# Kernel tuning notes

Measured on AMD Instinct MI355X. Metric: run time of the kernel, lower is better.

Reference implementation:

```python
import jax, jax.numpy as jnp
import numpy as np

B, N, CA, CS, CZ, H, NQ, NK = 2, 16384, 128, 128, 16, 4, 32, 128
DH = CA // H
NB = N // NQ


def _ln(x, gamma=None, eps=1e-5):
    m = jnp.mean(x, -1, keepdims=True)
    v = jnp.var(x, -1, keepdims=True)
    y = (x - m) * jax.lax.rsqrt(v + eps)
    return y if gamma is None else y * gamma


def _adaln(a, s, gamma_s, Wg, bg, Wskip):
    # AF3 Algorithm 26: LN(a) without affine; LN(s) with scale, no offset;
    # out = sigmoid(Linear(s)) * a + LinearNoBias(s)
    a_n = _ln(a)
    s_n = _ln(s, gamma_s)
    return jax.nn.sigmoid(s_n @ Wg + bg) * a_n + s_n @ Wskip


def setup_inputs():
    key = jax.random.key(0)
    ks = jax.random.split(key, 20)
    def nrm(i, shape, scale=0.02):
        return jax.random.normal(ks[i], shape, jnp.float32) * scale
    return {
        "a": jax.random.normal(ks[0], (B, N, CA), jnp.float32),
        "s": jax.random.normal(ks[1], (B, N, CS), jnp.float32),
        "z": jax.random.normal(ks[2], (B, NB, NQ, NK, CZ), jnp.float32),
        "apb_gamma_s": jnp.ones((CS,), jnp.float32),
        "apb_Wg": nrm(3, (CS, CA)),
        "apb_bg": jnp.zeros((CA,), jnp.float32),
        "apb_Wskip": nrm(4, (CS, CA)),
        "Wq": nrm(5, (CA, CA)), "bq": jnp.zeros((CA,), jnp.float32),
        "Wk": nrm(6, (CA, CA)), "Wv": nrm(7, (CA, CA)),
        "Wgate": nrm(8, (CA, CA)), "Wo": nrm(9, (CA, CA)),
        "gamma_z": jnp.ones((CZ,), jnp.float32),
        "Wz": nrm(10, (CZ, H)),
        "Ws_last": nrm(11, (CS, CA)),
        "bs_last": jnp.full((CA,), -2.0, jnp.float32),
        "ct_gamma_s": jnp.ones((CS,), jnp.float32),
        "ct_Wg": nrm(12, (CS, CA)), "ct_bg": jnp.zeros((CA,), jnp.float32),
        "ct_Wskip": nrm(13, (CS, CA)),
        "Wa1": nrm(14, (CA, 2 * CA)), "Wa2": nrm(15, (CA, 2 * CA)),
        "Wb": nrm(16, (2 * CA, CA)),
        "Ws": nrm(17, (CS, CA)), "bs": jnp.full((CA,), -2.0, jnp.float32),
        "n_queries": NQ, "n_keys": NK,
    }


def reference(a, s, z, apb_gamma_s, apb_Wg, apb_bg, apb_Wskip, Wq, bq, Wk, Wv,
              Wgate, Wo, gamma_z, Wz, Ws_last, bs_last, ct_gamma_s, ct_Wg,
              ct_bg, ct_Wskip, Wa1, Wa2, Wb, Ws, bs, n_queries, n_keys):
    nq, nk = int(n_queries), int(n_keys)
    nb = N // nq
    # ---- AttentionPairBias, local windowed attention ----
    a1 = _adaln(a, s, apb_gamma_s, apb_Wg, apb_bg, apb_Wskip)  # [B,N,CA]
    # trunked pair bias: [B,nb,nq,nk,H] -> [B,H,nb,nq,nk]
    bias = jnp.transpose(_ln(z, gamma_z) @ Wz, (0, 4, 1, 2, 3))
    q = (a1 @ Wq + bq).reshape(B, N, H, DH).transpose(0, 2, 1, 3)
    k = (a1 @ Wk).reshape(B, N, H, DH).transpose(0, 2, 1, 3)
    v = (a1 @ Wv).reshape(B, N, H, DH).transpose(0, 2, 1, 3)
    qb = q.reshape(B, H, nb, nq, DH)
    pad = (nk - nq) // 2
    # centered key window per query block
    idx = (jnp.arange(nb) * nq - pad)[:, None] + jnp.arange(nk)[None, :]  # [nb,nk]
    valid = (idx >= 0) & (idx < N)
    idxc = jnp.clip(idx, 0, N - 1)
    kb = k[:, :, idxc]  # [B,H,nb,nk,DH]
    vb = v[:, :, idxc]
    scores = jnp.einsum('bhnqd,bhnkd->bhnqk', qb, kb) / np.sqrt(DH).astype(np.float32) + bias
    scores = jnp.where(valid[None, None, :, None, :], scores, -1e9)
    attn = jax.nn.softmax(scores, axis=-1)
    o = jnp.einsum('bhnqk,bhnkd->bhnqd', attn, vb)  # [B,H,nb,nq,DH]
    o = o.reshape(B, H, N, DH).transpose(0, 2, 1, 3).reshape(B, N, CA)
    g = jax.nn.sigmoid(a1 @ Wgate)  # per-channel gating
    attn_out = (g * o) @ Wo
    b_out = jax.nn.sigmoid(s @ Ws_last + bs_last) * attn_out
    # ---- ConditionedTransitionBlock (Alg 25) ----
    a3 = _adaln(a, s, ct_gamma_s, ct_Wg, ct_bg, ct_Wskip)
    t = jax.nn.silu(a3 @ Wa1) * (a3 @ Wa2)
    ct_out = jax.nn.sigmoid(s @ Ws + bs) * (t @ Wb)
    # Alg 23: a = b + ConditionedTransitionBlock(a, s)
    return b_out + ct_out
```

## Files before the change

kernel.cpp:

```cpp
#include <hip/hip_runtime.h>

typedef _Float16 f16;
typedef f16 f16x8 __attribute__((ext_vector_type(8)));
typedef f16 f16x4 __attribute__((ext_vector_type(4)));
typedef f16 f16x2 __attribute__((ext_vector_type(2)));
typedef float f32x4 __attribute__((ext_vector_type(4)));

#define MFMA16(a,b,c) __builtin_amdgcn_mfma_f32_16x16x32_f16((a),(b),(c),0,0,0)

static __device__ __forceinline__ f16x8 ld8(const f16* p){ return *(const f16x8*)p; }
static __device__ __forceinline__ float sigm(float x){ return 1.f/(1.f + __expf(-x)); }

__global__ __launch_bounds__(256) void k_prep(
    const float* __restrict__ apb_gamma, const float* __restrict__ apb_Wg, const float* __restrict__ apb_Wskip,
    const float* __restrict__ ct_gamma,  const float* __restrict__ ct_Wg,  const float* __restrict__ ct_Wskip,
    const float* __restrict__ Wq, const float* __restrict__ Wk, const float* __restrict__ Wv, const float* __restrict__ Wgate,
    const float* __restrict__ Wsl, const float* __restrict__ Wss,
    const float* __restrict__ Wa1, const float* __restrict__ Wa2,
    const float* __restrict__ Wo, const float* __restrict__ Wb,
    const float* __restrict__ gamma_z, const float* __restrict__ Wz,
    f16* __restrict__ wA, f16* __restrict__ wC, f16* __restrict__ wQK, f16* __restrict__ wVG,
    f16* __restrict__ wSG, f16* __restrict__ wAB, f16* __restrict__ wO, f16* __restrict__ wBt,
    float* __restrict__ wzg, float* __restrict__ Slv, float* __restrict__ Ssv)
{
  const int t0 = blockIdx.x*256 + threadIdx.x;
  const int stride = gridDim.x*256;
  for (int i = t0; i < 256*128; i += stride){
    const int n = i >> 7, k = i & 127;
    const int m = n & 127;
    wA[i]  = (f16)(((n<128) ? apb_Wg[k*128+m] : apb_Wskip[k*128+m]) * apb_gamma[k]);
    wC[i]  = (f16)(((n<128) ? ct_Wg[k*128+m]  : ct_Wskip[k*128+m])  * ct_gamma[k]);
    wQK[i] = (f16)((n<128) ? Wq[k*128+m] : Wk[k*128+m]);
    wVG[i] = (f16)((n<128) ? Wv[k*128+m] : Wgate[k*128+m]);
    wSG[i] = (f16)((n<128) ? Wsl[k*128+m] : Wss[k*128+m]);
  }
  for (int i = t0; i < 512*128; i += stride){
    const int n = i >> 7, k = i & 127;
    wAB[i] = (f16)((n < 256) ? Wa1[k*256 + n] : Wa2[k*256 + (n-256)]);
  }
  for (int i = t0; i < 128*128; i += stride){
    const int n = i >> 7, k = i & 127;
    wO[i] = (f16)Wo[k*128+n];
  }
  for (int i = t0; i < 128*256; i += stride){
    const int n = i >> 8, k = i & 255;
    wBt[i] = (f16)Wb[k*128+n];
  }
  if (t0 < 64) wzg[t0] = gamma_z[t0 & 15] * Wz[(t0 & 15)*4 + (t0 >> 4)];
  if (t0 < 256){
    const int cc = t0 & 127;
    const float* Wp = (t0 >= 128) ? Wss : Wsl;
    float acc = 0.f;
    for (int k = 0; k < 128; k++) acc += Wp[k*128 + cc];
    if (t0 >= 128) Ssv[cc] = acc; else Slv[cc] = acc;
  }
}

__global__ __launch_bounds__(256) void k_pre(
    const float* __restrict__ A, const float* __restrict__ S,
    const f16* __restrict__ wA, const f16* __restrict__ wC,
    const f16* __restrict__ wQK, const f16* __restrict__ wVG,
    const f16* __restrict__ wSG, const f16* __restrict__ wAB,
    const float* __restrict__ bgA, const float* __restrict__ bgC,
    const float* __restrict__ bq, const float* __restrict__ bsl, const float* __restrict__ bss,
    const float* __restrict__ Slv, const float* __restrict__ Ssv,
    f16* __restrict__ Qo, f16* __restrict__ Ko, f16* __restrict__ Vt, f16* __restrict__ Go,
    f16* __restrict__ T, f16* __restrict__ GL, f16* __restrict__ GS)
{
  __shared__ f16 lsn[64*136];
  __shared__ f16 lan[64*136];
  __shared__ f16 la1[64*136];
  __shared__ f16 la3[64*136];
  __shared__ float lsm[64], lsd[64];
  const int tid = threadIdx.x;
  const size_t rbase = (size_t)blockIdx.x * 64;

  {
    const int row = tid >> 2, part = tid & 3;
    const size_t gr = rbase + row;
    {
      const float* sp = S + gr*128 + part*32;
      float v[32];
      #pragma unroll
      for (int j = 0; j < 8; j++){
        const float4 t4 = ((const float4*)sp)[j];
        v[j*4+0]=t4.x; v[j*4+1]=t4.y; v[j*4+2]=t4.z; v[j*4+3]=t4.w;
      }
      float sm = 0.f, sq = 0.f;
      #pragma unroll
      for (int j = 0; j < 32; j++){ sm += v[j]; sq += v[j]*v[j]; }
      sm += __shfl_xor(sm,1); sq += __shfl_xor(sq,1);
      sm += __shfl_xor(sm,2); sq += __shfl_xor(sq,2);
      const float mean = sm*(1.f/128.f);
      const float var  = sq*(1.f/128.f) - mean*mean;
      const float rstd = rsqrtf(var + 1e-5f);
      if (part == 0){ lsm[row] = mean; lsd[row] = (var + 1e-5f)*rstd; }
      #pragma unroll
      for (int j = 0; j < 4; j++){
        f16x8 o;
        #pragma unroll
        for (int e = 0; e < 8; e++) o[e] = (f16)((v[j*8+e]-mean)*rstd);
        *(f16x8*)&lsn[row*136 + part*32 + j*8] = o;
      }
    }
    {
      const float* ap = A + gr*128 + part*32;
      float v[32];
      #pragma unroll
      for (int j = 0; j < 8; j++){
        const float4 t4 = ((const float4*)ap)[j];
        v[j*4+0]=t4.x; v[j*4+1]=t4.y; v[j*4+2]=t4.z; v[j*4+3]=t4.w;
      }
      float sm = 0.f, sq = 0.f;
      #pragma unroll
      for (int j = 0; j < 32; j++){ sm += v[j]; sq += v[j]*v[j]; }
      sm += __shfl_xor(sm,1); sq += __shfl_xor(sq,1);
      sm += __shfl_xor(sm,2); sq += __shfl_xor(sq,2);
      const float mean = sm*(1.f/128.f);
      const float var  = sq*(1.f/128.f) - mean*mean;
      const float rstd = rsqrtf(var + 1e-5f);
      #pragma unroll
      for (int j = 0; j < 4; j++){
        f16x8 o;
        #pragma unroll
        for (int e = 0; e < 8; e++) o[e] = (f16)((v[j*8+e]-mean)*rstd);
        *(f16x8*)&lan[row*136 + part*32 + j*8] = o;
      }
    }
  }
  __syncthreads();

  const int l = tid & 63, w = tid >> 6;
  const int c = l & 15, q4 = l >> 4;

  for (int jj = 0; jj < 4; jj++){
    const int job = jj*4 + w;
    const int n0 = (job >> 1)*16;
    const int mat = job & 1;
    const f16* W = mat ? wC : wA;
    f16* dst = mat ? la3 : la1;
    const float bv = (mat ? bgC : bgA)[n0 + c];
    f16x8 b0[4], b1[4];
    #pragma unroll
    for (int kc = 0; kc < 4; kc++){
      b0[kc] = ld8(W + (size_t)(n0 + c)*128 + kc*32 + q4*8);
      b1[kc] = ld8(W + (size_t)(128 + n0 + c)*128 + kc*32 + q4*8);
    }
    for (int mi = 0; mi < 4; mi++){
      f32x4 d0 = {0,0,0,0}, d1 = {0,0,0,0};
      #pragma unroll
      for (int kc = 0; kc < 4; kc++){
        const f16x8 av = *(const f16x8*)&lsn[(mi*16 + c)*136 + kc*32 + q4*8];
        d0 = MFMA16(av, b0[kc], d0);
        d1 = MFMA16(av, b1[kc], d1);
      }
      #pragma unroll
      for (int r = 0; r < 4; r++){
        const int row = mi*16 + q4*4 + r;
        const float anv = (float)lan[row*136 + n0 + c];
        dst[row*136 + n0 + c] = (f16)(sigm(d0[r] + bv)*anv + d1[r]);
      }
    }
  }
  __syncthreads();

  for (int jj = 0; jj < 2; jj++){
    const int n0 = (jj*4 + w)*16;
    f16x8 bQ[4], bK[4], bV[4], bG[4];
    #pragma unroll
    for (int kc = 0; kc < 4; kc++){
      bQ[kc] = ld8(wQK + (size_t)(n0 + c)*128 + kc*32 + q4*8);
      bK[kc] = ld8(wQK + (size_t)(128 + n0 + c)*128 + kc*32 + q4*8);
      bV[kc] = ld8(wVG + (size_t)(n0 + c)*128 + kc*32 + q4*8);
      bG[kc] = ld8(wVG + (size_t)(128 + n0 + c)*128 + kc*32 + q4*8);
    }
    const float bvq = bq[n0 + c];
    for (int mi = 0; mi < 4; mi++){
      f32x4 dQ = {0,0,0,0}, dK = {0,0,0,0}, dV = {0,0,0,0}, dG = {0,0,0,0};
      #pragma unroll
      for (int kc = 0; kc < 4; kc++){
        const f16x8 av = *(const f16x8*)&la1[(mi*16 + c)*136 + kc*32 + q4*8];
        dQ = MFMA16(av, bQ[kc], dQ);
        dK = MFMA16(av, bK[kc], dK);
        dV = MFMA16(av, bV[kc], dV);
        dG = MFMA16(av, bG[kc], dG);
      }
      #pragma unroll
      for (int r = 0; r < 4; r++){
        const size_t grow = rbase + mi*16 + q4*4 + r;
        Qo[grow*128 + n0 + c] = (f16)((dQ[r] + bvq)*0.17677669529663687f);
        Ko[grow*128 + n0 + c] = (f16)dK[r];
        Go[grow*128 + n0 + c] = (f16)sigm(dG[r]);
      }
      f16x4 vv;
      #pragma unroll
      for (int r = 0; r < 4; r++) vv[r] = (f16)dV[r];
      const int bidx = (int)(rbase >> 14);
      const int ntk  = (int)(rbase & 16383) + mi*16 + q4*4;
      *(f16x4*)(Vt + ((size_t)bidx*128 + n0 + c)*16384 + ntk) = vv;
    }
  }

  for (int jj = 0; jj < 4; jj++){
    const int n0t = (jj*4 + w)*16;
    f16x8 b1v[4], b2v[4];
    #pragma unroll
    for (int kc = 0; kc < 4; kc++){
      b1v[kc] = ld8(wAB + (size_t)(n0t + c)*128 + kc*32 + q4*8);
      b2v[kc] = ld8(wAB + (size_t)(256 + n0t + c)*128 + kc*32 + q4*8);
    }
    for (int mi = 0; mi < 4; mi++){
      f32x4 d0 = {0,0,0,0}, d1 = {0,0,0,0};
      #pragma unroll
      for (int kc = 0; kc < 4; kc++){
        const f16x8 av = *(const f16x8*)&la3[(mi*16 + c)*136 + kc*32 + q4*8];
        d0 = MFMA16(av, b1v[kc], d0);
        d1 = MFMA16(av, b2v[kc], d1);
      }
      #pragma unroll
      for (int r = 0; r < 4; r++){
        const size_t grow = rbase + mi*16 + q4*4 + r;
        const float u = d0[r];
        T[grow*256 + n0t + c] = (f16)((u*sigm(u))*d1[r]);
      }
    }
  }

  for (int jj = 0; jj < 2; jj++){
    const int n0 = (jj*4 + w)*16;
    f16x8 b0[4], b1[4];
    #pragma unroll
    for (int kc = 0; kc < 4; kc++){
      b0[kc] = ld8(wSG + (size_t)(n0 + c)*128 + kc*32 + q4*8);
      b1[kc] = ld8(wSG + (size_t)(128 + n0 + c)*128 + kc*32 + q4*8);
    }
    const float slc = Slv[n0 + c], ssc = Ssv[n0 + c];
    const float bl = bsl[n0 + c],  bs2 = bss[n0 + c];
    for (int mi = 0; mi < 4; mi++){
      f32x4 d0 = {0,0,0,0}, d1 = {0,0,0,0};
      #pragma unroll
      for (int kc = 0; kc < 4; kc++){
        const f16x8 av = *(const f16x8*)&lsn[(mi*16 + c)*136 + kc*32 + q4*8];
        d0 = MFMA16(av, b0[kc], d0);
        d1 = MFMA16(av, b1[kc], d1);
      }
      #pragma unroll
      for (int r = 0; r < 4; r++){
        const int row = mi*16 + q4*4 + r;
        const size_t grow = rbase + row;
        const float mn = lsm[row], sd = lsd[row];
        GL[grow*128 + n0 + c] = (f16)sigm(d0[r]*sd + mn*slc + bl);
        GS[grow*128 + n0 + c] = (f16)sigm(d1[r]*sd + mn*ssc + bs2);
      }
    }
  }
}

__global__ __launch_bounds__(512) void k_attn(const f16* __restrict__ Q, const f16* __restrict__ K,
    const f16* __restrict__ VT, const float* __restrict__ Z, const float* __restrict__ WZG,
    f16* __restrict__ Og)
{
  __shared__ f16 upb[17408];
  __shared__ float wzg_s[64];
  const int tid = threadIdx.x;
  const int b = blockIdx.x >> 9, nb = blockIdx.x & 511;
  if (tid < 64) wzg_s[tid] = WZG[tid];
  __syncthreads();
  #pragma unroll
  for (int i = 0; i < 8; i++){
    const int p  = tid + i*512;
    const int qq = p >> 7, kk = p & 127;
    const float* zp = Z + ((((size_t)b*512 + nb)*32 + qq)*128 + kk)*16;
    const float4 z0 = *(const float4*)(zp);
    const float4 z1 = *(const float4*)(zp + 4);
    const float4 z2 = *(const float4*)(zp + 8);
    const float4 z3 = *(const float4*)(zp + 12);
    const float xs[16] = {z0.x,z0.y,z0.z,z0.w, z1.x,z1.y,z1.z,z1.w,
                          z2.x,z2.y,z2.z,z2.w, z3.x,z3.y,z3.z,z3.w};
    float sm = 0.f, sq = 0.f;
    #pragma unroll
    for (int cc = 0; cc < 16; cc++){ sm += xs[cc]; sq += xs[cc]*xs[cc]; }
    const float mean = sm*(1.f/16.f);
    const float var  = sq*(1.f/16.f) - mean*mean;
    const float rs   = rsqrtf(var + 1e-5f);
    #pragma unroll
    for (int h = 0; h < 4; h++){
      float acc = 0.f;
      #pragma unroll
      for (int cc = 0; cc < 16; cc++) acc += (xs[cc]-mean)*wzg_s[h*16+cc];
      upb[(h*32 + qq)*132 + kk] = (f16)(acc*rs);
    }
  }
  __syncthreads();

  const int l = tid & 63, w = tid >> 6;
  const int c = l & 15, q4 = l >> 4;
  const int h = w >> 1, qh = w & 1, m0 = qh*16;
  const f16x8 aq = ld8(Q + ((size_t)b*16384 + (size_t)nb*32 + m0 + c)*128 + h*32 + q4*8);
  const long kbase = (long)b*16384 + (long)nb*32 - 48;
  f32x4 sc[8];
  #pragma unroll
  for (int nt = 0; nt < 8; nt++){
    const f16x8 bf = ld8(K + (kbase + nt*16 + c)*128 + h*32 + q4*8);
    f32x4 zz = {0.f,0.f,0.f,0.f};
    sc[nt] = MFMA16(aq, bf, zz);
  }
  #pragma unroll
  for (int nt = 0; nt < 8; nt++){
    const int key = nt*16 + c;
    const long kt = (long)nb*32 - 48 + key;
    const bool inv = (kt < 0) || (kt >= 16384);
    #pragma unroll
    for (int r = 0; r < 4; r++){
      const float v = sc[nt][r] + (float)upb[(h*32 + m0 + q4*4 + r)*132 + key];
      sc[nt][r] = inv ? -1e9f : v;
    }
  }
  #pragma unroll
  for (int r = 0; r < 4; r++){
    float mx = sc[0][r];
    #pragma unroll
    for (int nt = 1; nt < 8; nt++) mx = fmaxf(mx, sc[nt][r]);
    #pragma unroll
    for (int o = 8; o; o >>= 1) mx = fmaxf(mx, __shfl_xor(mx, o));
    float sum = 0.f;
    #pragma unroll
    for (int nt = 0; nt < 8; nt++){ const float e = __expf(sc[nt][r]-mx); sc[nt][r] = e; sum += e; }
    #pragma unroll
    for (int o = 8; o; o >>= 1) sum += __shfl_xor(sum, o);
    const float inv = 1.f/sum;
    #pragma unroll
    for (int nt = 0; nt < 8; nt++) sc[nt][r] *= inv;
  }
  __syncthreads();
  #pragma unroll
  for (int nt = 0; nt < 8; nt++)
    #pragma unroll
    for (int r = 0; r < 4; r++)
      upb[(w*16 + q4*4 + r)*136 + nt*16 + c] = (f16)sc[nt][r];
  const f16* vb = VT + ((long)b*128)*16384 + (long)nb*32 - 48;
  f32x4 o0 = {0.f,0.f,0.f,0.f}, o1 = {0.f,0.f,0.f,0.f};
  #pragma unroll
  for (int kc = 0; kc < 4; kc++){
    const f16x8 pa = *(const f16x8*)&upb[(w*16 + c)*136 + kc*32 + q4*8];
    const f16x8 v0 = ld8(vb + (long)(h*32 + c)*16384 + kc*32 + q4*8);
    const f16x8 v1 = ld8(vb + (long)(h*32 + 16 + c)*16384 + kc*32 + q4*8);
    o0 = MFMA16(pa, v0, o0);
    o1 = MFMA16(pa, v1, o1);
  }
  #pragma unroll
  for (int r = 0; r < 4; r++){
    const size_t tok = (size_t)b*16384 + (size_t)nb*32 + m0 + q4*4 + r;
    Og[tok*128 + h*32 + c]      = (f16)o0[r];
    Og[tok*128 + h*32 + 16 + c] = (f16)o1[r];
  }
}

__global__ __launch_bounds__(256) void k_final(const f16* __restrict__ G, const f16* __restrict__ O,
    const f16* __restrict__ T, const f16* __restrict__ Wot, const f16* __restrict__ Wbt,
    const f16* __restrict__ GL, const f16* __restrict__ GS, float* __restrict__ out)
{
  const int l = threadIdx.x & 63, w = threadIdx.x >> 6;
  const int c = l & 15, q4 = l >> 4;
  const int mbase = blockIdx.x*64 + w*16;
  f16x8 ag[4], at[8];
  const f16* gp = G + (size_t)(mbase + c)*128 + q4*8;
  const f16* op = O + (size_t)(mbase + c)*128 + q4*8;
  #pragma unroll
  for (int kc = 0; kc < 4; kc++) ag[kc] = ld8(gp + kc*32) * ld8(op + kc*32);
  const f16* tp = T + (size_t)(mbase + c)*256 + q4*8;
  #pragma unroll
  for (int kc = 0; kc < 8; kc++) at[kc] = ld8(tp + kc*32);
  for (int nt = 0; nt < 8; nt++){
    const int cb = nt*16;
    f32x4 d1 = {0,0,0,0}, d2 = {0,0,0,0};
    #pragma unroll
    for (int kc = 0; kc < 4; kc++)
      d1 = MFMA16(ag[kc], ld8(Wot + (size_t)(cb + c)*128 + kc*32 + q4*8), d1);
    #pragma unroll
    for (int kc = 0; kc < 8; kc++)
      d2 = MFMA16(at[kc], ld8(Wbt + (size_t)(cb + c)*256 + kc*32 + q4*8), d2);
    #pragma unroll
    for (int r = 0; r < 4; r++){
      const size_t row = mbase + q4*4 + r;
      const float glv = (float)GL[row*128 + cb + c];
      const float gsv = (float)GS[row*128 + cb + c];
      out[row*128 + cb + c] = glv*d1[r] + gsv*d2[r];
    }
  }
}

extern "C" void kernel_launch(void* const* d_in, const int* in_sizes, int n_in,
                              void* d_out, int out_size, void* d_ws, size_t ws_size,
                              hipStream_t stream)
{
  (void)in_sizes; (void)n_in; (void)out_size; (void)ws_size;
  const float* a        = (const float*)d_in[0];
  const float* s        = (const float*)d_in[1];
  const float* z        = (const float*)d_in[2];
  const float* apb_gamma= (const float*)d_in[3];
  const float* apb_Wg   = (const float*)d_in[4];
  const float* apb_bg   = (const float*)d_in[5];
  const float* apb_Wskip= (const float*)d_in[6];
  const float* Wq       = (const float*)d_in[7];
  const float* bq       = (const float*)d_in[8];
  const float* Wk       = (const float*)d_in[9];
  const float* Wv       = (const float*)d_in[10];
  const float* Wgate    = (const float*)d_in[11];
  const float* Wo       = (const float*)d_in[12];
  const float* gamma_z  = (const float*)d_in[13];
  const float* Wz       = (const float*)d_in[14];
  const float* Wsl      = (const float*)d_in[15];
  const float* bsl      = (const float*)d_in[16];
  const float* ct_gamma = (const float*)d_in[17];
  const float* ct_Wg    = (const float*)d_in[18];
  const float* ct_bg    = (const float*)d_in[19];
  const float* ct_Wskip = (const float*)d_in[20];
  const float* Wa1      = (const float*)d_in[21];
  const float* Wa2      = (const float*)d_in[22];
  const float* Wb       = (const float*)d_in[23];
  const float* Wss      = (const float*)d_in[24];
  const float* bss      = (const float*)d_in[25];

  f16* W0 = (f16*)d_ws;
  const size_t SL = (size_t)32768*128;
  f16* qv = W0 + 0*SL;
  f16* kv = W0 + 1*SL;
  f16* vt = W0 + 2*SL;
  f16* gv = W0 + 3*SL;
  f16* tv = W0 + 4*SL;
  f16* gl = W0 + 6*SL;
  f16* gs = W0 + 7*SL;
  f16* ov = W0 + 8*SL;
  f16* wA  = W0 + 9*SL;
  f16* wC  = wA  + 256*128;
  f16* wQK = wC  + 256*128;
  f16* wVG = wQK + 256*128;
  f16* wSG = wVG + 256*128;
  f16* wAB = wSG + 256*128;
  f16* wO  = wAB + 512*128;
  f16* wBt = wO  + 128*128;
  float* wzg = (float*)(wBt + 128*256);
  float* Slv = wzg + 64;
  float* Ssv = Slv + 128;

  k_prep<<<dim3(64),256,0,stream>>>(apb_gamma,apb_Wg,apb_Wskip, ct_gamma,ct_Wg,ct_Wskip,
      Wq,Wk,Wv,Wgate, Wsl,Wss, Wa1,Wa2, Wo,Wb, gamma_z,Wz,
      wA,wC,wQK,wVG,wSG,wAB,wO,wBt,wzg,Slv,Ssv);
  k_pre<<<dim3(512),256,0,stream>>>(a,s, wA,wC,wQK,wVG,wSG,wAB,
      apb_bg,ct_bg,bq,bsl,bss,Slv,Ssv, qv,kv,vt,gv,tv,gl,gs);
  k_attn<<<dim3(1024),512,0,stream>>>(qv,kv,vt,z,wzg,ov);
  k_final<<<dim3(512),256,0,stream>>>(gv,ov,tv,wO,wBt,gl,gs,(float*)d_out);
}
```

Measured before the change: 534.9 us.

## Fuse output projection into attention kernel and trim k_pre shared memory

```diff
diff --git a/kernel.cpp b/kernel.cpp
--- a/kernel.cpp
+++ b/kernel.cpp
@@ -21,7 +21,8 @@
     const float* __restrict__ gamma_z, const float* __restrict__ Wz,
     f16* __restrict__ wA, f16* __restrict__ wC, f16* __restrict__ wQK, f16* __restrict__ wVG,
     f16* __restrict__ wSG, f16* __restrict__ wAB, f16* __restrict__ wO, f16* __restrict__ wBt,
-    float* __restrict__ wzg, float* __restrict__ Slv, float* __restrict__ Ssv)
+    float* __restrict__ wzg, float* __restrict__ Slv, float* __restrict__ Ssv,
+    float* __restrict__ wcs)
 {
   const int t0 = blockIdx.x*256 + threadIdx.x;
   const int stride = gridDim.x*256;
@@ -54,9 +55,14 @@
     for (int k = 0; k < 128; k++) acc += Wp[k*128 + cc];
     if (t0 >= 128) Ssv[cc] = acc; else Slv[cc] = acc;
   }
+  if (t0 < 4){
+    float acc = 0.f;
+    for (int cc = 0; cc < 16; cc++) acc += gamma_z[cc]*Wz[cc*4 + t0];
+    wcs[t0] = acc;
+  }
 }
 
-__global__ __launch_bounds__(256) void k_pre(
+__global__ __launch_bounds__(256,3) void k_pre(
     const float* __restrict__ A, const float* __restrict__ S,
     const f16* __restrict__ wA, const f16* __restrict__ wC,
     const f16* __restrict__ wQK, const f16* __restrict__ wVG,
@@ -67,10 +73,9 @@
     f16* __restrict__ Qo, f16* __restrict__ Ko, f16* __restrict__ Vt, f16* __restrict__ Go,
     f16* __restrict__ T, f16* __restrict__ GL, f16* __restrict__ GS)
 {
-  __shared__ f16 lsn[64*136];
-  __shared__ f16 lan[64*136];
-  __shared__ f16 la1[64*136];
-  __shared__ f16 la3[64*136];
+  __shared__ __attribute__((aligned(16))) f16 lsn[64*136];
+  __shared__ __attribute__((aligned(16))) f16 lan[64*136];
+  __shared__ __attribute__((aligned(16))) f16 la1[64*136];
   __shared__ float lsm[64], lsd[64];
   const int tid = threadIdx.x;
   const size_t rbase = (size_t)blockIdx.x * 64;
@@ -133,32 +138,33 @@
   const int l = tid & 63, w = tid >> 6;
   const int c = l & 15, q4 = l >> 4;
 
-  for (int jj = 0; jj < 4; jj++){
-    const int job = jj*4 + w;
-    const int n0 = (job >> 1)*16;
-    const int mat = job & 1;
-    const f16* W = mat ? wC : wA;
-    f16* dst = mat ? la3 : la1;
-    const float bv = (mat ? bgC : bgA)[n0 + c];
-    f16x8 b0[4], b1[4];
+  for (int jj = 0; jj < 2; jj++){
+    const int n0 = (jj*4 + w)*16;
+    const float bvA = bgA[n0 + c], bvC = bgC[n0 + c];
+    f16x8 bA0[4], bA1[4], bC0[4], bC1[4];
     #pragma unroll
     for (int kc = 0; kc < 4; kc++){
-      b0[kc] = ld8(W + (size_t)(n0 + c)*128 + kc*32 + q4*8);
-      b1[kc] = ld8(W + (size_t)(128 + n0 + c)*128 + kc*32 + q4*8);
+      bA0[kc] = ld8(wA + (size_t)(n0 + c)*128 + kc*32 + q4*8);
+      bA1[kc] = ld8(wA + (size_t)(128 + n0 + c)*128 + kc*32 + q4*8);
+      bC0[kc] = ld8(wC + (size_t)(n0 + c)*128 + kc*32 + q4*8);
+      bC1[kc] = ld8(wC + (size_t)(128 + n0 + c)*128 + kc*32 + q4*8);
     }
     for (int mi = 0; mi < 4; mi++){
-      f32x4 d0 = {0,0,0,0}, d1 = {0,0,0,0};
+      f32x4 dA0 = {0,0,0,0}, dA1 = {0,0,0,0}, dC0 = {0,0,0,0}, dC1 = {0,0,0,0};
       #pragma unroll
       for (int kc = 0; kc < 4; kc++){
         const f16x8 av = *(const f16x8*)&lsn[(mi*16 + c)*136 + kc*32 + q4*8];
-        d0 = MFMA16(av, b0[kc], d0);
-        d1 = MFMA16(av, b1[kc], d1);
+        dA0 = MFMA16(av, bA0[kc], dA0);
+        dA1 = MFMA16(av, bA1[kc], dA1);
+        dC0 = MFMA16(av, bC0[kc], dC0);
+        dC1 = MFMA16(av, bC1[kc], dC1);
       }
       #pragma unroll
       for (int r = 0; r < 4; r++){
         const int row = mi*16 + q4*4 + r;
         const float anv = (float)lan[row*136 + n0 + c];
-        dst[row*136 + n0 + c] = (f16)(sigm(d0[r] + bv)*anv + d1[r]);
+        la1[row*136 + n0 + c] = (f16)(sigm(dA0[r] + bvA)*anv + dA1[r]);
+        lan[row*136 + n0 + c] = (f16)(sigm(dC0[r] + bvC)*anv + dC1[r]);
       }
     }
   }
@@ -213,7 +219,7 @@
       f32x4 d0 = {0,0,0,0}, d1 = {0,0,0,0};
       #pragma unroll
       for (int kc = 0; kc < 4; kc++){
-        const f16x8 av = *(const f16x8*)&la3[(mi*16 + c)*136 + kc*32 + q4*8];
+        const f16x8 av = *(const f16x8*)&lan[(mi*16 + c)*136 + kc*32 + q4*8];
         d0 = MFMA16(av, b1v[kc], d0);
         d1 = MFMA16(av, b2v[kc], d1);
       }
@@ -256,15 +262,37 @@
   }
 }
 
-__global__ __launch_bounds__(512) void k_attn(const f16* __restrict__ Q, const f16* __restrict__ K,
+__global__ __launch_bounds__(512,2) void k_attn(const f16* __restrict__ Q, const f16* __restrict__ K,
     const f16* __restrict__ VT, const float* __restrict__ Z, const float* __restrict__ WZG,
-    f16* __restrict__ Og)
+    const float* __restrict__ WCS,
+    const f16* __restrict__ G, const f16* __restrict__ T,
+    const f16* __restrict__ GL, const f16* __restrict__ GS,
+    const f16* __restrict__ Wot, const f16* __restrict__ Wbt,
+    float* __restrict__ out)
 {
-  __shared__ f16 upb[17408];
+  __shared__ __attribute__((aligned(16))) f16 upb[17408];
+  __shared__ __attribute__((aligned(16))) f16 obuf[32*136];
   __shared__ float wzg_s[64];
+  __shared__ float wcs_s[4];
   const int tid = threadIdx.x;
   const int b = blockIdx.x >> 9, nb = blockIdx.x & 511;
   if (tid < 64) wzg_s[tid] = WZG[tid];
+  if (tid < 4)  wcs_s[tid] = WCS[tid];
+
+  const int l = tid & 63, w = tid >> 6;
+  const int c = l & 15, q4 = l >> 4;
+  const int h = w >> 1, qh = w & 1, m0 = qh*16;
+
+  const f16x8 aq = ld8(Q + ((size_t)b*16384 + (size_t)nb*32 + m0 + c)*128 + h*32 + q4*8);
+  const long kbase = (long)b*16384 + (long)nb*32 - 48;
+  f32x4 sc[8];
+  #pragma unroll
+  for (int nt = 0; nt < 8; nt++){
+    const f16x8 bf = ld8(K + (kbase + nt*16 + c)*128 + h*32 + q4*8);
+    f32x4 zz = {0.f,0.f,0.f,0.f};
+    sc[nt] = MFMA16(aq, bf, zz);
+  }
+
   __syncthreads();
   #pragma unroll
   for (int i = 0; i < 8; i++){
@@ -284,27 +312,15 @@
     const float var  = sq*(1.f/16.f) - mean*mean;
     const float rs   = rsqrtf(var + 1e-5f);
     #pragma unroll
-    for (int h = 0; h < 4; h++){
+    for (int hh = 0; hh < 4; hh++){
       float acc = 0.f;
       #pragma unroll
-      for (int cc = 0; cc < 16; cc++) acc += (xs[cc]-mean)*wzg_s[h*16+cc];
-      upb[(h*32 + qq)*132 + kk] = (f16)(acc*rs);
-    }
-  }
-  __syncthreads();
-
-  const int l = tid & 63, w = tid >> 6;
-  const int c = l & 15, q4 = l >> 4;
-  const int h = w >> 1, qh = w & 1, m0 = qh*16;
-  const f16x8 aq = ld8(Q + ((size_t)b*16384 + (size_t)nb*32 + m0 + c)*128 + h*32 + q4*8);
-  const long kbase = (long)b*16384 + (long)nb*32 - 48;
-  f32x4 sc[8];
-  #pragma unroll
-  for (int nt = 0; nt < 8; nt++){
-    const f16x8 bf = ld8(K + (kbase + nt*16 + c)*128 + h*32 + q4*8);
-    f32x4 zz = {0.f,0.f,0.f,0.f};
-    sc[nt] = MFMA16(aq, bf, zz);
-  }
+      for (int cc = 0; cc < 16; cc++) acc += xs[cc]*wzg_s[hh*16+cc];
+      upb[(hh*32 + qq)*132 + kk] = (f16)((acc - mean*wcs_s[hh])*rs);
+    }
+  }
+  __syncthreads();
+
   #pragma unroll
   for (int nt = 0; nt < 8; nt++){
     const int key = nt*16 + c;
@@ -338,6 +354,7 @@
     #pragma unroll
     for (int r = 0; r < 4; r++)
       upb[(w*16 + q4*4 + r)*136 + nt*16 + c] = (f16)sc[nt][r];
+
   const f16* vb = VT + ((long)b*128)*16384 + (long)nb*32 - 48;
   f32x4 o0 = {0.f,0.f,0.f,0.f}, o1 = {0.f,0.f,0.f,0.f};
   #pragma unroll
@@ -350,42 +367,37 @@
   }
   #pragma unroll
   for (int r = 0; r < 4; r++){
-    const size_t tok = (size_t)b*16384 + (size_t)nb*32 + m0 + q4*4 + r;
-    Og[tok*128 + h*32 + c]      = (f16)o0[r];
-    Og[tok*128 + h*32 + 16 + c] = (f16)o1[r];
-  }
-}
-
-__global__ __launch_bounds__(256) void k_final(const f16* __restrict__ G, const f16* __restrict__ O,
-    const f16* __restrict__ T, const f16* __restrict__ Wot, const f16* __restrict__ Wbt,
-    const f16* __restrict__ GL, const f16* __restrict__ GS, float* __restrict__ out)
-{
-  const int l = threadIdx.x & 63, w = threadIdx.x >> 6;
-  const int c = l & 15, q4 = l >> 4;
-  const int mbase = blockIdx.x*64 + w*16;
-  f16x8 ag[4], at[8];
-  const f16* gp = G + (size_t)(mbase + c)*128 + q4*8;
-  const f16* op = O + (size_t)(mbase + c)*128 + q4*8;
-  #pragma unroll
-  for (int kc = 0; kc < 4; kc++) ag[kc] = ld8(gp + kc*32) * ld8(op + kc*32);
-  const f16* tp = T + (size_t)(mbase + c)*256 + q4*8;
-  #pragma unroll
-  for (int kc = 0; kc < 8; kc++) at[kc] = ld8(tp + kc*32);
-  for (int nt = 0; nt < 8; nt++){
-    const int cb = nt*16;
+    obuf[(m0 + q4*4 + r)*136 + h*32 + c]      = (f16)o0[r];
+    obuf[(m0 + q4*4 + r)*136 + h*32 + 16 + c] = (f16)o1[r];
+  }
+  __syncthreads();
+
+  const int n0 = w*16;
+  f16x8 bo[4];
+  #pragma unroll
+  for (int kc = 0; kc < 4; kc++) bo[kc] = ld8(Wot + (size_t)(n0 + c)*128 + kc*32 + q4*8);
+  const size_t tok0 = (size_t)b*16384 + (size_t)nb*32;
+  #pragma unroll
+  for (int mt = 0; mt < 2; mt++){
+    const size_t arow = tok0 + mt*16 + c;
     f32x4 d1 = {0,0,0,0}, d2 = {0,0,0,0};
     #pragma unroll
-    for (int kc = 0; kc < 4; kc++)
-      d1 = MFMA16(ag[kc], ld8(Wot + (size_t)(cb + c)*128 + kc*32 + q4*8), d1);
-    #pragma unroll
-    for (int kc = 0; kc < 8; kc++)
-      d2 = MFMA16(at[kc], ld8(Wbt + (size_t)(cb + c)*256 + kc*32 + q4*8), d2);
+    for (int kc = 0; kc < 4; kc++){
+      const f16x8 av = ld8(G + arow*128 + kc*32 + q4*8) *
+                       *(const f16x8*)&obuf[(mt*16 + c)*136 + kc*32 + q4*8];
+      d1 = MFMA16(av, bo[kc], d1);
+    }
+    #pragma unroll
+    for (int kc = 0; kc < 8; kc++){
+      const f16x8 at = ld8(T + arow*256 + kc*32 + q4*8);
+      d2 = MFMA16(at, ld8(Wbt + (size_t)(n0 + c)*256 + kc*32 + q4*8), d2);
+    }
     #pragma unroll
     for (int r = 0; r < 4; r++){
-      const size_t row = mbase + q4*4 + r;
-      const float glv = (float)GL[row*128 + cb + c];
-      const float gsv = (float)GS[row*128 + cb + c];
-      out[row*128 + cb + c] = glv*d1[r] + gsv*d2[r];
+      const size_t row = tok0 + mt*16 + q4*4 + r;
+      const float glv = (float)GL[row*128 + n0 + c];
+      const float gsv = (float)GS[row*128 + n0 + c];
+      out[row*128 + n0 + c] = glv*d1[r] + gsv*d2[r];
     }
   }
 }
@@ -431,8 +443,7 @@
   f16* tv = W0 + 4*SL;
   f16* gl = W0 + 6*SL;
   f16* gs = W0 + 7*SL;
-  f16* ov = W0 + 8*SL;
-  f16* wA  = W0 + 9*SL;
+  f16* wA  = W0 + 8*SL;
   f16* wC  = wA  + 256*128;
   f16* wQK = wC  + 256*128;
   f16* wVG = wQK + 256*128;
@@ -443,12 +454,13 @@
   float* wzg = (float*)(wBt + 128*256);
   float* Slv = wzg + 64;
   float* Ssv = Slv + 128;
+  float* wcs = Ssv + 128;
 
   k_prep<<<dim3(64),256,0,stream>>>(apb_gamma,apb_Wg,apb_Wskip, ct_gamma,ct_Wg,ct_Wskip,
       Wq,Wk,Wv,Wgate, Wsl,Wss, Wa1,Wa2, Wo,Wb, gamma_z,Wz,
-      wA,wC,wQK,wVG,wSG,wAB,wO,wBt,wzg,Slv,Ssv);
+      wA,wC,wQK,wVG,wSG,wAB,wO,wBt,wzg,Slv,Ssv,wcs);
   k_pre<<<dim3(512),256,0,stream>>>(a,s, wA,wC,wQK,wVG,wSG,wAB,
       apb_bg,ct_bg,bq,bsl,bss,Slv,Ssv, qv,kv,vt,gv,tv,gl,gs);
-  k_attn<<<dim3(1024),512,0,stream>>>(qv,kv,vt,z,wzg,ov);
-  k_final<<<dim3(512),256,0,stream>>>(gv,ov,tv,wO,wBt,gl,gs,(float*)d_out);
+  k_attn<<<dim3(1024),512,0,stream>>>(qv,kv,vt,z,wzg,wcs, gv,tv,gl,gs, wO,wBt,
+      (float*)d_out);
 }
```

Measured after the change: 581.4 us. +8.7%, slower.
